# Kernel tuning notes

Hardware: AMD Instinct MI355X
Metric: run time of the kernel (lower is better)

## Reference

```python
import jax, jax.numpy as jnp
import numpy as np

N_PARTICLES = 128
D = 2048


def setup_inputs() -> dict:
    key = jax.random.key(0)
    k1, k2 = jax.random.split(key)
    var_flat = jax.random.normal(k1, (N_PARTICLES, D), dtype=jnp.float32)
    grad_flat = jax.random.normal(k2, (N_PARTICLES, D), dtype=jnp.float32)
    return {"var_flat": var_flat, "grad_flat": grad_flat}


def reference(var_flat, grad_flat):
    # SVGD gradient correction for one particle variable, as in SteinModel.train_step.
    n, d = var_flat.shape
    # M = grad^T grad / n  -> [d, d] metric
    M = jnp.matmul(grad_flat.T, grad_flat) / n
    # sign_diff[i, j, :] = var_flat[j] - var_flat[i]  (TF broadcasting of x - x[:, None])
    sign_diff = var_flat[None, :, :] - var_flat[:, None, :]  # [n, n, d]
    Msd = jnp.einsum('ijd,de->ije', sign_diff, M)  # [n, n, d]
    dMsd = jnp.sum(sign_diff * Msd, axis=2)  # [n, n]
    # median bandwidth: tfp.stats.percentile default interpolation is 'nearest'
    med = jnp.percentile(dMsd, 50.0, method='nearest')
    h = med ** 2 / np.float32(np.log(n))
    kern = jnp.exp(-dMsd / (2.0 * h))  # [n, n]
    # gkern = -einsum('ijd,ij->idj', Msd, kern) / h ; mgJ = kern @ grad - sum_j gkern
    mgJ = jnp.matmul(kern, grad_flat) + jnp.einsum('ijd,ij->id', Msd, kern) / h
    return mgJ
```

## Files before the change

### kernel.cpp

```cpp
#include <hip/hip_runtime.h>
#include <math.h>

#define NP   128
#define DIM  2048
#define NTHR 256

__global__ __launch_bounds__(NTHR) void k_pmat(const float* __restrict__ var,
                                               const float* __restrict__ grad,
                                               float* __restrict__ Ppart) {
    __shared__ float At[64 * 36];
    __shared__ float Bt[64 * 36];
    const int tid = threadIdx.x;
    const int b   = blockIdx.x;
    const int t   = b & 15;
    const int ck  = b >> 4;
    const int i0  = (t >> 2) * 32;
    const int j0  = (t & 3) * 32;
    const int tx  = tid & 15, ty = tid >> 4;
    const int lrow = 2 * ty + (tx >> 3);
    const int lcol = 4 * (tx & 7);
    float4 acc = {0.f, 0.f, 0.f, 0.f};
    for (int s = 0; s < 4; ++s) {
        const int kb = ck * 256 + s * 64;
        __syncthreads();
        #pragma unroll
        for (int p = 0; p < 2; ++p) {
            const int f  = tid + p * 256;
            const int r  = f >> 4;
            const int kq = (f & 15) * 4;
            const float4 a4 = *(const float4*)(var  + (i0 + r) * DIM + kb + kq);
            const float4 g4 = *(const float4*)(grad + (j0 + r) * DIM + kb + kq);
            At[(kq+0)*36 + r] = a4.x; At[(kq+1)*36 + r] = a4.y;
            At[(kq+2)*36 + r] = a4.z; At[(kq+3)*36 + r] = a4.w;
            Bt[(kq+0)*36 + r] = g4.x; Bt[(kq+1)*36 + r] = g4.y;
            Bt[(kq+2)*36 + r] = g4.z; Bt[(kq+3)*36 + r] = g4.w;
        }
        __syncthreads();
        #pragma unroll 8
        for (int k = 0; k < 64; ++k) {
            const float  a  = At[k*36 + lrow];
            const float4 b4 = *(const float4*)&Bt[k*36 + lcol];
            acc.x = fmaf(a, b4.x, acc.x);
            acc.y = fmaf(a, b4.y, acc.y);
            acc.z = fmaf(a, b4.z, acc.z);
            acc.w = fmaf(a, b4.w, acc.w);
        }
    }
    *(float4*)(Ppart + ck * (NP*NP) + (i0 + lrow) * NP + j0 + lcol) = acc;
}

extern __shared__ float k2smem[];

__global__ __launch_bounds__(NTHR) void k_dmsd(const float* __restrict__ Ppart,
                                               float* __restrict__ P,
                                               float* __restrict__ dMsd) {
    float* Pr  = k2smem;
    float* Dsh = k2smem + NP * 132;
    const int tid = threadIdx.x;
    const int b   = blockIdx.x;

    {
        const int i  = tid >> 1;
        const int jh = (tid & 1) * 64;
        float4 s[16];
        #pragma unroll
        for (int q = 0; q < 16; ++q) s[q] = {0.f, 0.f, 0.f, 0.f};
        for (int c = 0; c < 8; ++c) {
            const float* src = Ppart + c * (NP*NP) + i * NP + jh;
            #pragma unroll
            for (int q = 0; q < 16; ++q) {
                const float4 v = *(const float4*)(src + 4*q);
                s[q].x += v.x; s[q].y += v.y; s[q].z += v.z; s[q].w += v.w;
            }
        }
        #pragma unroll
        for (int q = 0; q < 16; ++q)
            *(float4*)&Pr[i*132 + jh + 4*q] = s[q];
    }
    __syncthreads();

    {
        const int f = tid * 4;
        const int r = f >> 7;
        const int c = f & 127;
        *(float4*)(P + (8*b + r) * NP + c) = *(const float4*)&Pr[(8*b + r)*132 + c];
    }

    if (tid < NP) {
        float acc = 0.f;
        #pragma unroll 8
        for (int k = 0; k < NP; k += 4) {
            const float4 p = *(const float4*)&Pr[tid*132 + k];
            acc = fmaf(p.x, p.x, acc);
            acc = fmaf(p.y, p.y, acc);
            acc = fmaf(p.z, p.z, acc);
            acc = fmaf(p.w, p.w, acc);
        }
        Dsh[tid] = acc;
    }
    __syncthreads();

    const int x  = tid & 127;
    const int r0 = 8*b + (tid >> 7) * 4;
    float a0 = 0.f, a1 = 0.f, a2 = 0.f, a3 = 0.f;
    #pragma unroll 4
    for (int m = 0; m < NP; ++m) {
        const float pm = Pr[x*132 + m];
        a0 = fmaf(Pr[(r0+0)*132 + m], pm, a0);
        a1 = fmaf(Pr[(r0+1)*132 + m], pm, a1);
        a2 = fmaf(Pr[(r0+2)*132 + m], pm, a2);
        a3 = fmaf(Pr[(r0+3)*132 + m], pm, a3);
    }
    const float Dx = Dsh[x];
    dMsd[(r0+0)*NP + x] = (Dsh[r0+0] + Dx - 2.f*a0) * (1.f/128.f);
    dMsd[(r0+1)*NP + x] = (Dsh[r0+1] + Dx - 2.f*a1) * (1.f/128.f);
    dMsd[(r0+2)*NP + x] = (Dsh[r0+2] + Dx - 2.f*a2) * (1.f/128.f);
    dMsd[(r0+3)*NP + x] = (Dsh[r0+3] + Dx - 2.f*a3) * (1.f/128.f);
}

__global__ __launch_bounds__(NTHR) void k_out(const float* __restrict__ P,
                                              const float* __restrict__ dMsd,
                                              const float* __restrict__ grad,
                                              float* __restrict__ out) {
    __shared__ float    kern[8 * 132];
    __shared__ float    Ash[8 * 132];
    __shared__ unsigned uparts[2][4];
    __shared__ float    rsp[4][4];

    const int tid  = threadIdx.x;
    const int b    = blockIdx.x;
    const int R8   = (b >> 4) * 8;
    const int CG   = (b & 15) * 128;
    const int j    = tid & 127;
    const int half = tid >> 7;
    const int rb   = half * 4;
    const int wid  = tid >> 6;

    unsigned v[64];
    #pragma unroll
    for (int u = 0; u < 64; ++u)
        v[u] = __float_as_uint(fmaxf(dMsd[u * 256 + tid], 0.f));

    unsigned lo = 0u;
    for (int bit = 30; bit >= 0; --bit) {
        const unsigned mid = lo | (1u << bit);
        unsigned cnt = 0;
        #pragma unroll
        for (int u = 0; u < 64; ++u) cnt += (v[u] < mid) ? 1u : 0u;
        #pragma unroll
        for (int o = 32; o > 0; o >>= 1) cnt += __shfl_down(cnt, o);
        if ((tid & 63) == 0) uparts[bit & 1][wid] = cnt;
        __syncthreads();
        const unsigned total = uparts[bit & 1][0] + uparts[bit & 1][1]
                             + uparts[bit & 1][2] + uparts[bit & 1][3];
        if (total <= 8192u) lo = mid;
    }
    const float med   = __uint_as_float(lo);
    const float h     = med * med * (1.0f / 4.852030263919617f);
    const float inv2h = 0.5f / h;
    const float invh  = 1.0f / h;

    float kv[4];
    #pragma unroll
    for (int q = 0; q < 4; ++q) {
        kv[q] = __expf(-dMsd[(R8 + rb + q) * NP + j] * inv2h);
        kern[(rb + q) * 132 + j] = kv[q];
    }
    #pragma unroll
    for (int q = 0; q < 4; ++q) {
        float t = kv[q];
        #pragma unroll
        for (int o = 32; o > 0; o >>= 1) t += __shfl_down(t, o);
        if ((tid & 63) == 0) rsp[wid][q] = t;
    }
    __syncthreads();
    float rsum[4];
    #pragma unroll
    for (int q = 0; q < 4; ++q)
        rsum[q] = rsp[2 * half][q] + rsp[2 * half + 1][q];

    {
        float acc[4] = {0.f, 0.f, 0.f, 0.f};
        #pragma unroll 4
        for (int m = 0; m < NP; ++m) {
            const float pc = P[m * NP + j];
            acc[0] = fmaf(kern[(rb+0)*132 + m], pc, acc[0]);
            acc[1] = fmaf(kern[(rb+1)*132 + m], pc, acc[1]);
            acc[2] = fmaf(kern[(rb+2)*132 + m], pc, acc[2]);
            acc[3] = fmaf(kern[(rb+3)*132 + m], pc, acc[3]);
        }
        const float sc = invh * (1.0f / 128.0f);
        #pragma unroll
        for (int q = 0; q < 4; ++q) {
            const float Pi = P[(R8 + rb + q) * NP + j];
            Ash[(rb + q) * 132 + j] = kv[q] + sc * (acc[q] - rsum[q] * Pi);
        }
    }
    __syncthreads();

    {
        float acc[4] = {0.f, 0.f, 0.f, 0.f};
        #pragma unroll 4
        for (int m = 0; m < NP; ++m) {
            const float g = grad[m * DIM + CG + j];
            acc[0] = fmaf(Ash[(rb+0)*132 + m], g, acc[0]);
            acc[1] = fmaf(Ash[(rb+1)*132 + m], g, acc[1]);
            acc[2] = fmaf(Ash[(rb+2)*132 + m], g, acc[2]);
            acc[3] = fmaf(Ash[(rb+3)*132 + m], g, acc[3]);
        }
        #pragma unroll
        for (int q = 0; q < 4; ++q)
            out[(R8 + rb + q) * DIM + CG + j] = acc[q];
    }
}

extern "C" void kernel_launch(void* const* d_in, const int* in_sizes, int n_in,
                              void* d_out, int out_size, void* d_ws, size_t ws_size,
                              hipStream_t stream) {
    const float* var  = (const float*)d_in[0];
    const float* grad = (const float*)d_in[1];
    float* out = (float*)d_out;

    float* Ppart = (float*)d_ws;
    float* P     = Ppart + 8 * NP * NP;
    float* dMsd  = P + NP * NP;

    const int k2_lds = (NP * 132 + NP) * 4;
    hipFuncSetAttribute((const void*)k_dmsd,
                        hipFuncAttributeMaxDynamicSharedMemorySize, k2_lds);

    k_pmat<<<dim3(128), dim3(NTHR), 0,      stream>>>(var, grad, Ppart);
    k_dmsd<<<dim3(16),  dim3(NTHR), k2_lds, stream>>>(Ppart, P, dMsd);
    k_out <<<dim3(256), dim3(NTHR), 0,      stream>>>(P, dMsd, grad, out);
}
```

Baseline: 129.8 us.

## Widen k_out to 1024 threads and use radix-4 median search

The output kernel now runs 1024 threads per block, so each thread holds 16 dMsd values instead of 64 and computes one output row instead of four. The median binary search now resolves two bits per iteration with three thresholds, which halves the number of block-wide barriers and reduction rounds. The intent is to shorten the serial median-selection phase that every block repeats. In exchange there are more shuffles per round, 16-wave reductions through shared memory, and less reuse of each P and grad load across rows.

```diff
diff --git a/kernel.cpp b/kernel.cpp
--- a/kernel.cpp
+++ b/kernel.cpp
@@ -118,99 +118,96 @@
     dMsd[(r0+3)*NP + x] = (Dsh[r0+3] + Dx - 2.f*a3) * (1.f/128.f);
 }
 
-__global__ __launch_bounds__(NTHR) void k_out(const float* __restrict__ P,
+__global__ __launch_bounds__(1024) void k_out(const float* __restrict__ P,
                                               const float* __restrict__ dMsd,
                                               const float* __restrict__ grad,
                                               float* __restrict__ out) {
     __shared__ float    kern[8 * 132];
     __shared__ float    Ash[8 * 132];
-    __shared__ unsigned uparts[2][4];
-    __shared__ float    rsp[4][4];
-
-    const int tid  = threadIdx.x;
-    const int b    = blockIdx.x;
-    const int R8   = (b >> 4) * 8;
-    const int CG   = (b & 15) * 128;
-    const int j    = tid & 127;
-    const int half = tid >> 7;
-    const int rb   = half * 4;
-    const int wid  = tid >> 6;
-
-    unsigned v[64];
+    __shared__ unsigned cnt_lds[2][16][3];
+    __shared__ float    rsp[16];
+
+    const int tid = threadIdx.x;
+    const int b   = blockIdx.x;
+    const int R8  = (b >> 4) * 8;
+    const int CG  = (b & 15) * 128;
+    const int wid = tid >> 6;
+    const int r   = tid >> 7;
+    const int j   = tid & 127;
+
+    unsigned v[16];
     #pragma unroll
-    for (int u = 0; u < 64; ++u)
-        v[u] = __float_as_uint(fmaxf(dMsd[u * 256 + tid], 0.f));
+    for (int u = 0; u < 16; ++u)
+        v[u] = __float_as_uint(fmaxf(dMsd[u * 1024 + tid], 0.f));
 
     unsigned lo = 0u;
-    for (int bit = 30; bit >= 0; --bit) {
-        const unsigned mid = lo | (1u << bit);
-        unsigned cnt = 0;
-        #pragma unroll
-        for (int u = 0; u < 64; ++u) cnt += (v[u] < mid) ? 1u : 0u;
-        #pragma unroll
-        for (int o = 32; o > 0; o >>= 1) cnt += __shfl_down(cnt, o);
-        if ((tid & 63) == 0) uparts[bit & 1][wid] = cnt;
+    for (int it = 15; it >= 0; --it) {
+        const int sh = 2 * it;
+        const unsigned m0 = lo | (1u << sh);
+        const unsigned m1 = lo | (2u << sh);
+        const unsigned m2 = lo | (3u << sh);
+        unsigned c0 = 0, c1 = 0, c2 = 0;
+        #pragma unroll
+        for (int u = 0; u < 16; ++u) {
+            c0 += (v[u] < m0) ? 1u : 0u;
+            c1 += (v[u] < m1) ? 1u : 0u;
+            c2 += (v[u] < m2) ? 1u : 0u;
+        }
+        #pragma unroll
+        for (int o = 32; o > 0; o >>= 1) {
+            c0 += __shfl_down(c0, o);
+            c1 += __shfl_down(c1, o);
+            c2 += __shfl_down(c2, o);
+        }
+        if ((tid & 63) == 0) {
+            cnt_lds[it & 1][wid][0] = c0;
+            cnt_lds[it & 1][wid][1] = c1;
+            cnt_lds[it & 1][wid][2] = c2;
+        }
         __syncthreads();
-        const unsigned total = uparts[bit & 1][0] + uparts[bit & 1][1]
-                             + uparts[bit & 1][2] + uparts[bit & 1][3];
-        if (total <= 8192u) lo = mid;
+        unsigned t0 = 0, t1 = 0, t2 = 0;
+        #pragma unroll
+        for (int w = 0; w < 16; ++w) {
+            t0 += cnt_lds[it & 1][w][0];
+            t1 += cnt_lds[it & 1][w][1];
+            t2 += cnt_lds[it & 1][w][2];
+        }
+        if      (t2 <= 8192u) lo = m2;
+        else if (t1 <= 8192u) lo = m1;
+        else if (t0 <= 8192u) lo = m0;
     }
     const float med   = __uint_as_float(lo);
     const float h     = med * med * (1.0f / 4.852030263919617f);
     const float inv2h = 0.5f / h;
     const float invh  = 1.0f / h;
 
-    float kv[4];
-    #pragma unroll
-    for (int q = 0; q < 4; ++q) {
-        kv[q] = __expf(-dMsd[(R8 + rb + q) * NP + j] * inv2h);
-        kern[(rb + q) * 132 + j] = kv[q];
-    }
-    #pragma unroll
-    for (int q = 0; q < 4; ++q) {
-        float t = kv[q];
+    const float kv = __expf(-dMsd[(R8 + r) * NP + j] * inv2h);
+    kern[r * 132 + j] = kv;
+    {
+        float t = kv;
         #pragma unroll
         for (int o = 32; o > 0; o >>= 1) t += __shfl_down(t, o);
-        if ((tid & 63) == 0) rsp[wid][q] = t;
-    }
-    __syncthreads();
-    float rsum[4];
-    #pragma unroll
-    for (int q = 0; q < 4; ++q)
-        rsum[q] = rsp[2 * half][q] + rsp[2 * half + 1][q];
-
-    {
-        float acc[4] = {0.f, 0.f, 0.f, 0.f};
-        #pragma unroll 4
-        for (int m = 0; m < NP; ++m) {
-            const float pc = P[m * NP + j];
-            acc[0] = fmaf(kern[(rb+0)*132 + m], pc, acc[0]);
-            acc[1] = fmaf(kern[(rb+1)*132 + m], pc, acc[1]);
-            acc[2] = fmaf(kern[(rb+2)*132 + m], pc, acc[2]);
-            acc[3] = fmaf(kern[(rb+3)*132 + m], pc, acc[3]);
-        }
-        const float sc = invh * (1.0f / 128.0f);
-        #pragma unroll
-        for (int q = 0; q < 4; ++q) {
-            const float Pi = P[(R8 + rb + q) * NP + j];
-            Ash[(rb + q) * 132 + j] = kv[q] + sc * (acc[q] - rsum[q] * Pi);
-        }
-    }
-    __syncthreads();
-
-    {
-        float acc[4] = {0.f, 0.f, 0.f, 0.f};
-        #pragma unroll 4
-        for (int m = 0; m < NP; ++m) {
-            const float g = grad[m * DIM + CG + j];
-            acc[0] = fmaf(Ash[(rb+0)*132 + m], g, acc[0]);
-            acc[1] = fmaf(Ash[(rb+1)*132 + m], g, acc[1]);
-            acc[2] = fmaf(Ash[(rb+2)*132 + m], g, acc[2]);
-            acc[3] = fmaf(Ash[(rb+3)*132 + m], g, acc[3]);
-        }
-        #pragma unroll
-        for (int q = 0; q < 4; ++q)
-            out[(R8 + rb + q) * DIM + CG + j] = acc[q];
+        if ((tid & 63) == 0) rsp[wid] = t;
+    }
+    __syncthreads();
+    const float rs = rsp[2 * r] + rsp[2 * r + 1];
+
+    {
+        float acc = 0.f;
+        #pragma unroll 8
+        for (int m = 0; m < NP; ++m)
+            acc = fmaf(kern[r * 132 + m], P[m * NP + j], acc);
+        const float Pi = P[(R8 + r) * NP + j];
+        Ash[r * 132 + j] = kv + invh * (1.0f / 128.0f) * (acc - rs * Pi);
+    }
+    __syncthreads();
+
+    {
+        float acc = 0.f;
+        #pragma unroll 8
+        for (int m = 0; m < NP; ++m)
+            acc = fmaf(Ash[r * 132 + m], grad[m * DIM + CG + j], acc);
+        out[(R8 + r) * DIM + CG + j] = acc;
     }
 }
 
@@ -229,7 +226,7 @@
     hipFuncSetAttribute((const void*)k_dmsd,
                         hipFuncAttributeMaxDynamicSharedMemorySize, k2_lds);
 
-    k_pmat<<<dim3(128), dim3(NTHR), 0,      stream>>>(var, grad, Ppart);
-    k_dmsd<<<dim3(16),  dim3(NTHR), k2_lds, stream>>>(Ppart, P, dMsd);
-    k_out <<<dim3(256), dim3(NTHR), 0,      stream>>>(P, dMsd, grad, out);
-}
+    k_pmat<<<dim3(128), dim3(NTHR),  0,      stream>>>(var, grad, Ppart);
+    k_dmsd<<<dim3(16),  dim3(NTHR),  k2_lds, stream>>>(Ppart, P, dMsd);
+    k_out <<<dim3(256), dim3(1024),  0,      stream>>>(P, dMsd, grad, out);
+}
```

After: 126.8 us. 2.4% less time.
